# Kernel optimization log

Hardware: AMD Instinct MI355X
Metric: run time of the kernel (lower is better)

## Reference

```python
import jax, jax.numpy as jnp
import numpy as np

B, D, H = 32768, 1024, 8
LN_EPS = 1e-5


def setup_inputs() -> dict:
    key = jax.random.key(0)
    ks = jax.random.split(key, 12)
    w = lambda k, shape: (jax.random.normal(k, shape, dtype=jnp.float32) * 0.02)
    inp = {
        "graph_embedding": jax.random.normal(ks[0], (B, D), dtype=jnp.float32),
        "smiles_embedding": jax.random.normal(ks[1], (B, D), dtype=jnp.float32),
        "num_heads": H,
        # cross_attn_graph_to_smiles params (torch MHA: in_proj [3D,D] split q/k/v, out_proj [D,D])
        "Wq_gs": w(ks[2], (D, D)), "Wk_gs": w(ks[3], (D, D)), "Wv_gs": w(ks[4], (D, D)),
        "bq_gs": jnp.zeros((D,), jnp.float32), "bk_gs": jnp.zeros((D,), jnp.float32), "bv_gs": jnp.zeros((D,), jnp.float32),
        "Wo_gs": w(ks[5], (D, D)), "bo_gs": jnp.zeros((D,), jnp.float32),
        # cross_attn_smiles_to_graph params
        "Wq_sg": w(ks[6], (D, D)), "Wk_sg": w(ks[7], (D, D)), "Wv_sg": w(ks[8], (D, D)),
        "bq_sg": jnp.zeros((D,), jnp.float32), "bk_sg": jnp.zeros((D,), jnp.float32), "bv_sg": jnp.zeros((D,), jnp.float32),
        "Wo_sg": w(ks[9], (D, D)), "bo_sg": jnp.zeros((D,), jnp.float32),
        # LayerNorms
        "ln_g_gamma": jnp.ones((D,), jnp.float32), "ln_g_beta": jnp.zeros((D,), jnp.float32),
        "ln_s_gamma": jnp.ones((D,), jnp.float32), "ln_s_beta": jnp.zeros((D,), jnp.float32),
        # Gate: Linear(2D -> D) then sigmoid
        "Wg": w(ks[10], (D, 2 * D)), "bg": jnp.zeros((D,), jnp.float32),
    }
    return inp


def _layernorm(x, gamma, beta):
    mu = jnp.mean(x, axis=-1, keepdims=True)
    var = jnp.mean(jnp.square(x - mu), axis=-1, keepdims=True)
    return (x - mu) * jax.lax.rsqrt(var + LN_EPS) * gamma + beta


def _mha_len1(kv, Wv, bv, Wo, bo):
    # seq_len=1 cross-attention: softmax over a single key is identically 1,
    # so output == out_proj(v_proj(kv)). q/k projections contribute nothing
    # (and have exactly zero gradient), matching torch's math.
    v = kv @ Wv.T + bv
    return v @ Wo.T + bo


def reference(graph_embedding, smiles_embedding, num_heads,
              Wq_gs, Wk_gs, Wv_gs, bq_gs, bk_gs, bv_gs, Wo_gs, bo_gs,
              Wq_sg, Wk_sg, Wv_sg, bq_sg, bk_sg, bv_sg, Wo_sg, bo_sg,
              ln_g_gamma, ln_g_beta, ln_s_gamma, ln_s_beta, Wg, bg):
    # dropout p=0 / eval mode -> identity
    attn_g2s = _mha_len1(smiles_embedding, Wv_gs, bv_gs, Wo_gs, bo_gs)  # graph queries smiles
    attn_s2g = _mha_len1(graph_embedding, Wv_sg, bv_sg, Wo_sg, bo_sg)   # smiles queries graph
    fused_graph = _layernorm(graph_embedding + attn_g2s, ln_g_gamma, ln_g_beta)
    fused_smiles = _layernorm(smiles_embedding + attn_s2g, ln_s_gamma, ln_s_beta)
    gate_in = jnp.concatenate([fused_graph, fused_smiles], axis=1)  # [B, 2D]
    gate_weight = jax.nn.sigmoid(gate_in @ Wg.T + bg)               # [B, D]
    fused_feature = gate_weight * fused_graph + (1.0 - gate_weight) * fused_smiles
    return fused_feature, gate_weight
```

## Files before the change

kernel.cpp:

```cpp
#include <hip/hip_runtime.h>

#define BROWS 32768
#define DDIM 1024

typedef __bf16 bf16x8v __attribute__((ext_vector_type(8)));
typedef float f32x4v __attribute__((ext_vector_type(4)));

__device__ __forceinline__ float bf2f(unsigned short u) {
  union { unsigned int i; float f; } w; w.i = ((unsigned int)u) << 16; return w.f;
}
__device__ __forceinline__ unsigned short f2bf(float f) {
  union { float f; unsigned int i; } w; w.f = f;
  w.i += 0x7fffu + ((w.i >> 16) & 1u);
  return (unsigned short)(w.i >> 16);
}

__device__ __forceinline__ void gl_lds16(const void* g, void* l) {
  __builtin_amdgcn_global_load_lds((const __attribute__((address_space(1))) void*)g,
                                   (__attribute__((address_space(3))) void*)l, 16, 0, 0);
}

__device__ __forceinline__ int xcd_swz(int bid, int nwg) {
  return (bid & 7) * (nwg >> 3) + (bid >> 3);
}

__device__ __forceinline__ int swzc(int row, int col) {
  return (col & ~63) | ((col & 63) ^ ((row & 7) << 3));
}

__global__ __launch_bounds__(256) void cvt_x(const float* __restrict__ g,
                                             const float* __restrict__ s,
                                             unsigned short* __restrict__ xg,
                                             unsigned short* __restrict__ xs) {
  const size_t N = (size_t)BROWS * DDIM;
  size_t i = ((size_t)blockIdx.x * 256 + threadIdx.x) * 4;
  const float* src = (i < N) ? g : s;
  unsigned short* dst = (i < N) ? xg : xs;
  size_t off = (i < N) ? i : i - N;
  int row = (int)(off >> 10), col = (int)(off & 1023);
  float4 v = *(const float4*)&src[off];
  union { uint2 q; unsigned short h[4]; } u;
  u.h[0] = f2bf(v.x); u.h[1] = f2bf(v.y); u.h[2] = f2bf(v.z); u.h[3] = f2bf(v.w);
  *(uint2*)&dst[(size_t)row * DDIM + swzc(row, col)] = u.q;
}

__global__ __launch_bounds__(256) void cvt_wg(const float* __restrict__ s,
                                              unsigned short* __restrict__ d) {
  int i = (blockIdx.x * 256 + threadIdx.x) * 4;
  int row = i >> 11, col = i & 2047;
  float4 v = *(const float4*)&s[i];
  union { uint2 q; unsigned short h[4]; } u;
  u.h[0] = f2bf(v.x); u.h[1] = f2bf(v.y); u.h[2] = f2bf(v.z); u.h[3] = f2bf(v.w);
  *(uint2*)&d[(size_t)row * 2048 + swzc(row, col)] = u.q;
}

__global__ __launch_bounds__(256) void bias_combine(
    const float* __restrict__ Wo_gs, const float* __restrict__ bv_gs,
    const float* __restrict__ bo_gs,
    const float* __restrict__ Wo_sg, const float* __restrict__ bv_sg,
    const float* __restrict__ bo_sg,
    float* __restrict__ bc_gs, float* __restrict__ bc_sg) {
  int gid = blockIdx.x * 256 + threadIdx.x;
  int pair = gid >> 10, j = gid & 1023;
  const float* Wo = pair ? Wo_sg : Wo_gs;
  const float* bv = pair ? bv_sg : bv_gs;
  const float* bo = pair ? bo_sg : bo_gs;
  float s = 0.f;
  for (int k = 0; k < DDIM; k += 4) {
    float4 w = *(const float4*)&Wo[(size_t)j * DDIM + k];
    float4 b = *(const float4*)&bv[k];
    s += w.x * b.x + w.y * b.y + w.z * b.z + w.w * b.w;
  }
  float* bc = pair ? bc_sg : bc_gs;
  bc[j] = s + bo[j];
}

__device__ __forceinline__ void stage_f32_32(const float* __restrict__ src, int ldk,
                                             int row0, int k0, unsigned short* lds, int tid) {
  const int sr = tid >> 2, sc = (tid & 3) * 8;
#pragma unroll
  for (int h = 0; h < 2; ++h) {
    const float* g = &src[(size_t)(row0 + h * 64 + sr) * ldk + k0 + sc];
    float4 va = ((const float4*)g)[0];
    float4 vb = ((const float4*)g)[1];
    union { uint4 q; unsigned short hh[8]; } u;
    u.hh[0] = f2bf(va.x); u.hh[1] = f2bf(va.y); u.hh[2] = f2bf(va.z); u.hh[3] = f2bf(va.w);
    u.hh[4] = f2bf(vb.x); u.hh[5] = f2bf(vb.y); u.hh[6] = f2bf(vb.z); u.hh[7] = f2bf(vb.w);
    *(uint4*)&lds[(h * 64 + sr) * 32 + sc] = u.q;
  }
}

__device__ __forceinline__ void mfma_tile32(const unsigned short* As, const unsigned short* Bs,
                                            int ab, int bb, f32x4v acc[4][4]) {
  const bf16x8v* Av = reinterpret_cast<const bf16x8v*>(As);
  const bf16x8v* Bv = reinterpret_cast<const bf16x8v*>(Bs);
  bf16x8v af[4], bfr[4];
#pragma unroll
  for (int m = 0; m < 4; ++m) af[m] = Av[ab + m * 64];
#pragma unroll
  for (int n = 0; n < 4; ++n) bfr[n] = Bv[bb + n * 64];
#pragma unroll
  for (int m = 0; m < 4; ++m)
#pragma unroll
    for (int n = 0; n < 4; ++n)
      acc[m][n] = __builtin_amdgcn_mfma_f32_16x16x32_bf16(af[m], bfr[n], acc[m][n], 0, 0, 0);
}

__global__ __launch_bounds__(256) void combine_kernel(
    const float* __restrict__ Wo_gs, const float* __restrict__ Wv_gs,
    const float* __restrict__ Wo_sg, const float* __restrict__ Wv_sg,
    unsigned short* __restrict__ Wc_gs, unsigned short* __restrict__ Wc_sg) {
  const int pair = blockIdx.y;
  const float* Wo = pair ? Wo_sg : Wo_gs;
  const float* Wv = pair ? Wv_sg : Wv_gs;
  unsigned short* Wc = pair ? Wc_sg : Wc_gs;
  const int mt = blockIdx.x >> 3, nt = blockIdx.x & 7;
  const int row0 = mt * 128, col0 = nt * 128;

  __shared__ __align__(16) unsigned short As[128 * 32];
  __shared__ __align__(16) unsigned short Bt[128 * 32];

  const int tid = threadIdx.x;
  const int lane = tid & 63, wave = tid >> 6;
  const int wr = wave >> 1, wc = wave & 1;
  const int lr = lane & 15, lk = lane >> 4;

  f32x4v acc[4][4] = {};
  const int ab = (wr * 64 + lr) * 4 + lk;
  const int bb = (wc * 64 + lr) * 4 + lk;

  for (int tt = 0; tt < 32; ++tt) {
    const int t0 = tt * 32;
    __syncthreads();
    stage_f32_32(Wo, DDIM, row0, t0, As, tid);
#pragma unroll
    for (int h = 0; h < 2; ++h) {
      int chunk = h * 256 + tid;
      int t = chunk >> 4;
      int c8 = (chunk & 15) * 8;
      const float* g = &Wv[(size_t)(t0 + t) * DDIM + col0 + c8];
      float4 va = ((const float4*)g)[0];
      float4 vb = ((const float4*)g)[1];
      float vv[8] = {va.x, va.y, va.z, va.w, vb.x, vb.y, vb.z, vb.w};
#pragma unroll
      for (int e = 0; e < 8; ++e) Bt[(c8 + e) * 32 + t] = f2bf(vv[e]);
    }
    __syncthreads();
    mfma_tile32(As, Bt, ab, bb, acc);
  }

#pragma unroll
  for (int n = 0; n < 4; ++n) {
    int col = col0 + wc * 64 + n * 16 + lr;
#pragma unroll
    for (int m = 0; m < 4; ++m) {
      int rbase = row0 + wr * 64 + m * 16 + lk * 4;
#pragma unroll
      for (int r = 0; r < 4; ++r)
        Wc[(size_t)(rbase + r) * DDIM + swzc(rbase + r, col)] = f2bf(acc[m][n][r]);
    }
  }
}


__global__ __launch_bounds__(512, 2) void gemm_branch8(
    const unsigned short* __restrict__ Xs_b, const unsigned short* __restrict__ Xg_b,
    const unsigned short* __restrict__ Wc_gs, const unsigned short* __restrict__ Wc_sg,
    const float* __restrict__ bc_gs, const float* __restrict__ bc_sg,
    unsigned short* __restrict__ Zg, unsigned short* __restrict__ Zs) {
  const int pair = blockIdx.y;
  const unsigned short* X = pair ? Xg_b : Xs_b;
  const unsigned short* residb = pair ? Xs_b : Xg_b;
  const unsigned short* Wc = pair ? Wc_sg : Wc_gs;
  const float* bc = pair ? bc_sg : bc_gs;
  unsigned short* Z = pair ? Zs : Zg;

  const int bid = xcd_swz(blockIdx.x, 1024);
  const int mt = bid >> 2, nt = bid & 3;
  const int row0 = mt * 128, col0 = nt * 256;
  const int NT = 16;

  __shared__ __align__(16) unsigned short As[4][128 * 64];
  __shared__ __align__(16) unsigned short Bs[2][256 * 64];

  const int tid = threadIdx.x;
  const int lane = tid & 63, wave = tid >> 6;
  const int wm = wave >> 2, wn = wave & 3;
  const int lr = lane & 15, lk = lane >> 4;

  f32x4v acc[4][4] = {};

  auto stageB = [&](int kt, int jj) {
    int idx = jj * 512 + tid, row = idx >> 3, ch = idx & 7;
    gl_lds16(&Wc[(size_t)(col0 + row) * DDIM + kt * 64 + ch * 8], &Bs[kt & 1][idx * 8]);
  };
  auto stageA = [&](int kt, int jj) {
    int idx = jj * 512 + tid, row = idx >> 3, ch = idx & 7;
    gl_lds16(&X[(size_t)(row0 + row) * DDIM + kt * 64 + ch * 8], &As[kt & 3][idx * 8]);
  };

  stageB(0, 0); stageB(0, 1); stageB(0, 2); stageB(0, 3);
  stageA(0, 0); stageA(0, 1);
  stageA(1, 0); stageA(1, 1);
  stageA(2, 0); stageA(2, 1);
  asm volatile("s_waitcnt vmcnt(4)" ::: "memory");
  asm volatile("s_barrier" ::: "memory");

  for (int kt = 0; kt < NT; ++kt) {
    const unsigned short* Ak = As[kt & 3];
    const unsigned short* Bk = Bs[kt & 1];
    bf16x8v bv[4][2];
    {
      bf16x8v av[2][2];
#pragma unroll
      for (int mi = 0; mi < 2; ++mi)
#pragma unroll
        for (int s = 0; s < 2; ++s) {
          int row = wm * 64 + mi * 16 + lr;
          av[mi][s] = *(const bf16x8v*)&Ak[row * 64 + (((s * 4 + lk) ^ (row & 7)) * 8)];
        }
#pragma unroll
      for (int n = 0; n < 4; ++n)
#pragma unroll
        for (int s = 0; s < 2; ++s) {
          int row = wn * 64 + n * 16 + lr;
          bv[n][s] = *(const bf16x8v*)&Bk[row * 64 + (((s * 4 + lk) ^ (row & 7)) * 8)];
        }
      if (kt + 1 < NT) { stageB(kt + 1, 0); stageB(kt + 1, 1); stageB(kt + 1, 2); }
      asm volatile("s_barrier" ::: "memory");
      __builtin_amdgcn_s_setprio(1);
#pragma unroll
      for (int mi = 0; mi < 2; ++mi)
#pragma unroll
        for (int n = 0; n < 4; ++n)
#pragma unroll
          for (int s = 0; s < 2; ++s)
            acc[mi][n] = __builtin_amdgcn_mfma_f32_16x16x32_bf16(av[mi][s], bv[n][s],
                                                                 acc[mi][n], 0, 0, 0);
      __builtin_amdgcn_s_setprio(0);
      asm volatile("s_barrier" ::: "memory");
    }
    {
      bf16x8v av[2][2];
#pragma unroll
      for (int mi = 0; mi < 2; ++mi)
#pragma unroll
        for (int s = 0; s < 2; ++s) {
          int row = wm * 64 + (2 + mi) * 16 + lr;
          av[mi][s] = *(const bf16x8v*)&Ak[row * 64 + (((s * 4 + lk) ^ (row & 7)) * 8)];
        }
      if (kt + 1 < NT) stageB(kt + 1, 3);
      if (kt + 3 < NT) {
        stageA(kt + 3, 0); stageA(kt + 3, 1);
        asm volatile("s_waitcnt vmcnt(2)" ::: "memory");
      } else {
        asm volatile("s_waitcnt vmcnt(0)" ::: "memory");
      }
      asm volatile("s_barrier" ::: "memory");
      __builtin_amdgcn_s_setprio(1);
#pragma unroll
      for (int mi = 0; mi < 2; ++mi)
#pragma unroll
        for (int n = 0; n < 4; ++n)
#pragma unroll
          for (int s = 0; s < 2; ++s)
            acc[2 + mi][n] = __builtin_amdgcn_mfma_f32_16x16x32_bf16(av[mi][s], bv[n][s],
                                                                     acc[2 + mi][n], 0, 0, 0);
      __builtin_amdgcn_s_setprio(0);
      asm volatile("s_barrier" ::: "memory");
    }
  }

#pragma unroll
  for (int n = 0; n < 4; ++n) {
    int col = col0 + wn * 64 + n * 16 + lr;
    float bcv = bc[col];
#pragma unroll
    for (int m = 0; m < 4; ++m) {
      int rb = row0 + wm * 64 + m * 16 + lk * 4;
#pragma unroll
      for (int r = 0; r < 4; ++r) {
        int row = rb + r;
        size_t idx = (size_t)row * DDIM + swzc(row, col);
        Z[idx] = f2bf(acc[m][n][r] + bcv + bf2f(residb[idx]));
      }
    }
  }
}

__global__ __launch_bounds__(512, 2) void gemm_gate8(
    const unsigned short* __restrict__ fg, const unsigned short* __restrict__ fs,
    const unsigned short* __restrict__ WgB, const float* __restrict__ bg,
    float* __restrict__ out0, float* __restrict__ out1) {
  const int bid = xcd_swz(blockIdx.x, 1024);
  const int mt = bid >> 2, nt = bid & 3;
  const int row0 = mt * 128, col0 = nt * 256;
  const int NT = 32;

  __shared__ __align__(16) unsigned short As[4][128 * 64];
  __shared__ __align__(16) unsigned short Bs[2][256 * 64];

  const int tid = threadIdx.x;
  const int lane = tid & 63, wave = tid >> 6;
  const int wm = wave >> 2, wn = wave & 3;
  const int lr = lane & 15, lk = lane >> 4;

  f32x4v acc[4][4] = {};

  auto stageB = [&](int kt, int jj) {
    int idx = jj * 512 + tid, row = idx >> 3, ch = idx & 7;
    gl_lds16(&WgB[(size_t)(col0 + row) * 2048 + kt * 64 + ch * 8], &Bs[kt & 1][idx * 8]);
  };
  auto stageA = [&](int kt, int jj) {
    const unsigned short* asrc = (kt < 16) ? fg : fs;
    int ak0 = (kt & 15) * 64;
    int idx = jj * 512 + tid, row = idx >> 3, ch = idx & 7;
    gl_lds16(&asrc[(size_t)(row0 + row) * DDIM + ak0 + ch * 8], &As[kt & 3][idx * 8]);
  };

  stageB(0, 0); stageB(0, 1); stageB(0, 2); stageB(0, 3);
  stageA(0, 0); stageA(0, 1);
  stageA(1, 0); stageA(1, 1);
  stageA(2, 0); stageA(2, 1);
  asm volatile("s_waitcnt vmcnt(4)" ::: "memory");
  asm volatile("s_barrier" ::: "memory");

  for (int kt = 0; kt < NT; ++kt) {
    const unsigned short* Ak = As[kt & 3];
    const unsigned short* Bk = Bs[kt & 1];
    bf16x8v bv[4][2];
    {
      bf16x8v av[2][2];
#pragma unroll
      for (int mi = 0; mi < 2; ++mi)
#pragma unroll
        for (int s = 0; s < 2; ++s) {
          int row = wm * 64 + mi * 16 + lr;
          av[mi][s] = *(const bf16x8v*)&Ak[row * 64 + (((s * 4 + lk) ^ (row & 7)) * 8)];
        }
#pragma unroll
      for (int n = 0; n < 4; ++n)
#pragma unroll
        for (int s = 0; s < 2; ++s) {
          int row = wn * 64 + n * 16 + lr;
          bv[n][s] = *(const bf16x8v*)&Bk[row * 64 + (((s * 4 + lk) ^ (row & 7)) * 8)];
        }
      if (kt + 1 < NT) { stageB(kt + 1, 0); stageB(kt + 1, 1); stageB(kt + 1, 2); }
      asm volatile("s_barrier" ::: "memory");
      __builtin_amdgcn_s_setprio(1);
#pragma unroll
      for (int mi = 0; mi < 2; ++mi)
#pragma unroll
        for (int n = 0; n < 4; ++n)
#pragma unroll
          for (int s = 0; s < 2; ++s)
            acc[mi][n] = __builtin_amdgcn_mfma_f32_16x16x32_bf16(av[mi][s], bv[n][s],
                                                                 acc[mi][n], 0, 0, 0);
      __builtin_amdgcn_s_setprio(0);
      asm volatile("s_barrier" ::: "memory");
    }
    {
      bf16x8v av[2][2];
#pragma unroll
      for (int mi = 0; mi < 2; ++mi)
#pragma unroll
        for (int s = 0; s < 2; ++s) {
          int row = wm * 64 + (2 + mi) * 16 + lr;
          av[mi][s] = *(const bf16x8v*)&Ak[row * 64 + (((s * 4 + lk) ^ (row & 7)) * 8)];
        }
      if (kt + 1 < NT) stageB(kt + 1, 3);
      if (kt + 3 < NT) {
        stageA(kt + 3, 0); stageA(kt + 3, 1);
        asm volatile("s_waitcnt vmcnt(2)" ::: "memory");
      } else {
        asm volatile("s_waitcnt vmcnt(0)" ::: "memory");
      }
      asm volatile("s_barrier" ::: "memory");
      __builtin_amdgcn_s_setprio(1);
#pragma unroll
      for (int mi = 0; mi < 2; ++mi)
#pragma unroll
        for (int n = 0; n < 4; ++n)
#pragma unroll
          for (int s = 0; s < 2; ++s)
            acc[2 + mi][n] = __builtin_amdgcn_mfma_f32_16x16x32_bf16(av[mi][s], bv[n][s],
                                                                     acc[2 + mi][n], 0, 0, 0);
      __builtin_amdgcn_s_setprio(0);
      asm volatile("s_barrier" ::: "memory");
    }
  }

#pragma unroll
  for (int n = 0; n < 4; ++n) {
    int col = col0 + wn * 64 + n * 16 + lr;
    float bgv = bg[col];
#pragma unroll
    for (int m = 0; m < 4; ++m) {
      int rb = row0 + wm * 64 + m * 16 + lk * 4;
#pragma unroll
      for (int r = 0; r < 4; ++r) {
        int row = rb + r;
        size_t sidx = (size_t)row * DDIM + swzc(row, col);
        size_t tidx = (size_t)row * DDIM + col;
        float g = 1.f / (1.f + __expf(-(acc[m][n][r] + bgv)));
        float a = bf2f(fg[sidx]), b = bf2f(fs[sidx]);
        out0[tidx] = g * a + (1.f - g) * b;
        out1[tidx] = g;
      }
    }
  }
}

__global__ __launch_bounds__(256) void ln_kernel(
    unsigned short* __restrict__ Z,
    const float* __restrict__ gam_g, const float* __restrict__ bet_g,
    const float* __restrict__ gam_s, const float* __restrict__ bet_s) {
  int row = blockIdx.x * 4 + (threadIdx.x >> 6);
  int lane = threadIdx.x & 63;
  const float* gam = (row < BROWS) ? gam_g : gam_s;
  const float* bet = (row < BROWS) ? bet_g : bet_s;
  unsigned short* zr = Z + (size_t)row * DDIM;

  uint4 v0 = *(const uint4*)(zr + lane * 8);
  uint4 v1 = *(const uint4*)(zr + 512 + lane * 8);
  const unsigned short* u0 = (const unsigned short*)&v0;
  const unsigned short* u1 = (const unsigned short*)&v1;
  float x[16];
  float s = 0.f, sq = 0.f;
#pragma unroll
  for (int e = 0; e < 8; ++e) { x[e] = bf2f(u0[e]); x[8 + e] = bf2f(u1[e]); }
#pragma unroll
  for (int i = 0; i < 16; ++i) { s += x[i]; sq += x[i] * x[i]; }
#pragma unroll
  for (int o = 32; o; o >>= 1) { s += __shfl_xor(s, o); sq += __shfl_xor(sq, o); }
  float mu = s * (1.f / 1024.f);
  float var = sq * (1.f / 1024.f) - mu * mu;
  float rstd = rsqrtf(var + 1e-5f);

  int lane2 = (lane & ~7) | ((lane & 7) ^ (row & 7));
  float4 g0 = *(const float4*)(gam + lane2 * 8);
  float4 g1 = *(const float4*)(gam + lane2 * 8 + 4);
  float4 g2 = *(const float4*)(gam + 512 + lane2 * 8);
  float4 g3 = *(const float4*)(gam + 512 + lane2 * 8 + 4);
  float4 b0 = *(const float4*)(bet + lane2 * 8);
  float4 b1 = *(const float4*)(bet + lane2 * 8 + 4);
  float4 b2 = *(const float4*)(bet + 512 + lane2 * 8);
  float4 b3 = *(const float4*)(bet + 512 + lane2 * 8 + 4);
  float gg[16] = {g0.x,g0.y,g0.z,g0.w,g1.x,g1.y,g1.z,g1.w,
                  g2.x,g2.y,g2.z,g2.w,g3.x,g3.y,g3.z,g3.w};
  float bb[16] = {b0.x,b0.y,b0.z,b0.w,b1.x,b1.y,b1.z,b1.w,
                  b2.x,b2.y,b2.z,b2.w,b3.x,b3.y,b3.z,b3.w};

  union { uint4 q; unsigned short h[8]; } o0, o1;
#pragma unroll
  for (int e = 0; e < 8; ++e) {
    o0.h[e] = f2bf((x[e] - mu) * rstd * gg[e] + bb[e]);
    o1.h[e] = f2bf((x[8 + e] - mu) * rstd * gg[8 + e] + bb[8 + e]);
  }
  *(uint4*)(zr + lane * 8) = o0.q;
  *(uint4*)(zr + 512 + lane * 8) = o1.q;
}

__global__ __launch_bounds__(256) void gemm_gate_f32(
    const unsigned short* __restrict__ fg, const unsigned short* __restrict__ fs,
    const float* __restrict__ Wg, const float* __restrict__ bg,
    float* __restrict__ out0, float* __restrict__ out1) {
  const int bid = xcd_swz(blockIdx.x, 2048);
  const int mt = bid >> 3, nt = bid & 7;
  const int row0 = mt * 128, col0 = nt * 128;

  __shared__ __align__(16) unsigned short As[128 * 64];
  __shared__ __align__(16) unsigned short Bsh[128 * 64];

  const int tid = threadIdx.x;
  const int lane = tid & 63, wave = tid >> 6;
  const int wr = wave >> 1, wc = wave & 1;
  const int lr = lane & 15, lk = lane >> 4;

  f32x4v acc[4][4] = {};

  for (int kt = 0; kt < 32; ++kt) {
    const unsigned short* Asrc = (kt < 16) ? fg : fs;
    const int k0 = (kt & 15) * 64;
    const int kw = kt * 64;
    __syncthreads();
#pragma unroll
    for (int h = 0; h < 4; ++h) {
      int row = h * 32 + (tid >> 3);
      gl_lds16(&Asrc[(size_t)(row0 + row) * DDIM + k0 + (tid & 7) * 8], &As[h * 2048 + tid * 8]);
    }
#pragma unroll
    for (int h = 0; h < 4; ++h) {
      int row = h * 32 + (tid >> 3), c16 = tid & 7;
      const float* gsrc = &Wg[(size_t)(col0 + row) * 2048 + kw + c16 * 8];
      float4 va = ((const float4*)gsrc)[0];
      float4 vb = ((const float4*)gsrc)[1];
      union { uint4 q; unsigned short hh[8]; } u;
      u.hh[0] = f2bf(va.x); u.hh[1] = f2bf(va.y); u.hh[2] = f2bf(va.z); u.hh[3] = f2bf(va.w);
      u.hh[4] = f2bf(vb.x); u.hh[5] = f2bf(vb.y); u.hh[6] = f2bf(vb.z); u.hh[7] = f2bf(vb.w);
      *(uint4*)&Bsh[(row * 8 + (c16 ^ (row & 7))) * 8] = u.q;
    }
    __syncthreads();
    const bf16x8v* Av = reinterpret_cast<const bf16x8v*>(As);
    const bf16x8v* Bv = reinterpret_cast<const bf16x8v*>(Bsh);
    const int xr = lr & 7;
#pragma unroll
    for (int s = 0; s < 2; ++s) {
      const int u = (s * 4 + lk) ^ xr;
      bf16x8v af[4], bfr[4];
#pragma unroll
      for (int m = 0; m < 4; ++m) af[m] = Av[(wr * 64 + m * 16 + lr) * 8 + u];
#pragma unroll
      for (int n = 0; n < 4; ++n) bfr[n] = Bv[(wc * 64 + n * 16 + lr) * 8 + u];
#pragma unroll
      for (int m = 0; m < 4; ++m)
#pragma unroll
        for (int n = 0; n < 4; ++n)
          acc[m][n] = __builtin_amdgcn_mfma_f32_16x16x32_bf16(af[m], bfr[n], acc[m][n], 0, 0, 0);
    }
  }

#pragma unroll
  for (int n = 0; n < 4; ++n) {
    int col = col0 + wc * 64 + n * 16 + lr;
    float bgv = bg[col];
#pragma unroll
    for (int m = 0; m < 4; ++m) {
      int rbase = row0 + wr * 64 + m * 16 + lk * 4;
#pragma unroll
      for (int r = 0; r < 4; ++r) {
        int row = rbase + r;
        size_t sidx = (size_t)row * DDIM + swzc(row, col);
        size_t tidx = (size_t)row * DDIM + col;
        float g = 1.f / (1.f + __expf(-(acc[m][n][r] + bgv)));
        float a = bf2f(fg[sidx]), b = bf2f(fs[sidx]);
        out0[tidx] = g * a + (1.f - g) * b;
        out1[tidx] = g;
      }
    }
  }
}

extern "C" void kernel_launch(void* const* d_in, const int* in_sizes, int n_in,
                              void* d_out, int out_size, void* d_ws, size_t ws_size,
                              hipStream_t stream) {
  const float* graph  = (const float*)d_in[0];
  const float* smiles = (const float*)d_in[1];
  const float* Wv_gs  = (const float*)d_in[5];
  const float* bv_gs  = (const float*)d_in[8];
  const float* Wo_gs  = (const float*)d_in[9];
  const float* bo_gs  = (const float*)d_in[10];
  const float* Wv_sg  = (const float*)d_in[13];
  const float* bv_sg  = (const float*)d_in[16];
  const float* Wo_sg  = (const float*)d_in[17];
  const float* bo_sg  = (const float*)d_in[18];
  const float* ln_gg  = (const float*)d_in[19];
  const float* ln_gb  = (const float*)d_in[20];
  const float* ln_sg  = (const float*)d_in[21];
  const float* ln_sb  = (const float*)d_in[22];
  const float* Wg     = (const float*)d_in[23];
  const float* bg     = (const float*)d_in[24];

  char* ob = (char*)d_out;
  unsigned short* Xg_b  = (unsigned short*)ob;
  unsigned short* Xs_b  = (unsigned short*)(ob + (64u << 20));
  unsigned short* Wc_gs = (unsigned short*)(ob + (128u << 20));
  unsigned short* Wc_sg = (unsigned short*)(ob + (130u << 20));
  float* bc_gs = (float*)(ob + (132u << 20));
  float* bc_sg = (float*)(ob + (132u << 20) + 4096);

  unsigned short* Zg = (unsigned short*)d_ws;
  unsigned short* Zs = Zg + (size_t)BROWS * DDIM;
  const bool fast = ws_size >= ((size_t)132 << 20);
  unsigned short* WgB = (unsigned short*)((char*)d_ws + ((size_t)128 << 20));

  float* out0 = (float*)d_out;
  float* out1 = out0 + (size_t)BROWS * DDIM;

  cvt_x<<<dim3(65536), dim3(256), 0, stream>>>(graph, smiles, Xg_b, Xs_b);
  bias_combine<<<dim3(8), dim3(256), 0, stream>>>(Wo_gs, bv_gs, bo_gs, Wo_sg, bv_sg, bo_sg,
                                                  bc_gs, bc_sg);
  combine_kernel<<<dim3(64, 2), dim3(256), 0, stream>>>(Wo_gs, Wv_gs, Wo_sg, Wv_sg,
                                                        Wc_gs, Wc_sg);
  if (fast) cvt_wg<<<dim3(2048), dim3(256), 0, stream>>>(Wg, WgB);
  gemm_branch8<<<dim3(1024, 2), dim3(512), 0, stream>>>(Xs_b, Xg_b, Wc_gs, Wc_sg,
                                                        bc_gs, bc_sg, Zg, Zs);
  ln_kernel<<<dim3(16384), dim3(256), 0, stream>>>(Zg, ln_gg, ln_gb, ln_sg, ln_sb);
  if (fast)
    gemm_gate8<<<dim3(1024), dim3(512), 0, stream>>>(Zg, Zs, WgB, bg, out0, out1);
  else
    gemm_gate_f32<<<dim3(2048), dim3(256), 0, stream>>>(Zg, Zs, Wg, bg, out0, out1);
}
```

Baseline: 756.1 us.

## Enlarge GEMM tiles to 256x256 with double-buffered A and four-phase pipeline

Both bf16 GEMM kernels (branch and gate) move from 128x256 to 256x256 output tiles per block, halving the grid and doubling the accumulators per wave. The A buffer changes from a 4-deep 128-row ring to a 2-deep 256-row ring. B fragments are now loaded once per k-step, and the loop is split into four phases that interleave next-step B and A loads with MFMA work. The aim is more reuse per global byte and fewer redundant B loads. In exchange, register pressure rises (32 accumulators per lane) under launch_bounds(512,2), which may cause spills or lower occupancy, and prefetch depth is shallower.

```diff
diff --git a/kernel.cpp b/kernel.cpp
--- a/kernel.cpp
+++ b/kernel.cpp
@@ -163,6 +163,7 @@
 }
 
 
+
 __global__ __launch_bounds__(512, 2) void gemm_branch8(
     const unsigned short* __restrict__ Xs_b, const unsigned short* __restrict__ Xg_b,
     const unsigned short* __restrict__ Wc_gs, const unsigned short* __restrict__ Wc_sg,
@@ -175,12 +176,12 @@
   const float* bc = pair ? bc_sg : bc_gs;
   unsigned short* Z = pair ? Zs : Zg;
 
-  const int bid = xcd_swz(blockIdx.x, 1024);
+  const int bid = xcd_swz(blockIdx.x, 512);
   const int mt = bid >> 2, nt = bid & 3;
-  const int row0 = mt * 128, col0 = nt * 256;
+  const int row0 = mt * 256, col0 = nt * 256;
   const int NT = 16;
 
-  __shared__ __align__(16) unsigned short As[4][128 * 64];
+  __shared__ __align__(16) unsigned short As[2][256 * 64];
   __shared__ __align__(16) unsigned short Bs[2][256 * 64];
 
   const int tid = threadIdx.x;
@@ -188,45 +189,54 @@
   const int wm = wave >> 2, wn = wave & 3;
   const int lr = lane & 15, lk = lane >> 4;
 
-  f32x4v acc[4][4] = {};
-
+  f32x4v acc[8][4] = {};
+
+  auto stageA = [&](int kt, int jj) {
+    int idx = jj * 512 + tid, row = idx >> 3, ch = idx & 7;
+    gl_lds16(&X[(size_t)(row0 + row) * DDIM + kt * 64 + ch * 8], &As[kt & 1][idx * 8]);
+  };
   auto stageB = [&](int kt, int jj) {
     int idx = jj * 512 + tid, row = idx >> 3, ch = idx & 7;
     gl_lds16(&Wc[(size_t)(col0 + row) * DDIM + kt * 64 + ch * 8], &Bs[kt & 1][idx * 8]);
   };
-  auto stageA = [&](int kt, int jj) {
-    int idx = jj * 512 + tid, row = idx >> 3, ch = idx & 7;
-    gl_lds16(&X[(size_t)(row0 + row) * DDIM + kt * 64 + ch * 8], &As[kt & 3][idx * 8]);
-  };
 
   stageB(0, 0); stageB(0, 1); stageB(0, 2); stageB(0, 3);
-  stageA(0, 0); stageA(0, 1);
-  stageA(1, 0); stageA(1, 1);
-  stageA(2, 0); stageA(2, 1);
-  asm volatile("s_waitcnt vmcnt(4)" ::: "memory");
+  stageA(0, 0); stageA(0, 2);
+  stageA(0, 1); stageA(0, 3);
+  asm volatile("s_waitcnt vmcnt(2)" ::: "memory");
   asm volatile("s_barrier" ::: "memory");
 
   for (int kt = 0; kt < NT; ++kt) {
-    const unsigned short* Ak = As[kt & 3];
+    const unsigned short* Ak = As[kt & 1];
     const unsigned short* Bk = Bs[kt & 1];
     bf16x8v bv[4][2];
-    {
+#pragma unroll
+    for (int n = 0; n < 4; ++n)
+#pragma unroll
+      for (int s = 0; s < 2; ++s) {
+        int row = wn * 64 + n * 16 + lr;
+        bv[n][s] = *(const bf16x8v*)&Bk[row * 64 + (((s * 4 + lk) ^ (row & 7)) * 8)];
+      }
+#pragma unroll
+    for (int ph = 0; ph < 4; ++ph) {
       bf16x8v av[2][2];
 #pragma unroll
       for (int mi = 0; mi < 2; ++mi)
 #pragma unroll
         for (int s = 0; s < 2; ++s) {
-          int row = wm * 64 + mi * 16 + lr;
+          int row = wm * 128 + (ph * 2 + mi) * 16 + lr;
           av[mi][s] = *(const bf16x8v*)&Ak[row * 64 + (((s * 4 + lk) ^ (row & 7)) * 8)];
         }
-#pragma unroll
-      for (int n = 0; n < 4; ++n)
-#pragma unroll
-        for (int s = 0; s < 2; ++s) {
-          int row = wn * 64 + n * 16 + lr;
-          bv[n][s] = *(const bf16x8v*)&Bk[row * 64 + (((s * 4 + lk) ^ (row & 7)) * 8)];
-        }
-      if (kt + 1 < NT) { stageB(kt + 1, 0); stageB(kt + 1, 1); stageB(kt + 1, 2); }
+      if (kt + 1 < NT) {
+        if (ph == 0) { stageB(kt + 1, 0); stageB(kt + 1, 1); }
+        else if (ph == 1) { stageB(kt + 1, 2); stageB(kt + 1, 3);
+                            asm volatile("s_waitcnt vmcnt(4)" ::: "memory"); }
+        else if (ph == 2) { stageA(kt + 1, 0); stageA(kt + 1, 2); }
+        else { stageA(kt + 1, 1); stageA(kt + 1, 3);
+               asm volatile("s_waitcnt vmcnt(2)" ::: "memory"); }
+      } else {
+        if (ph == 1) asm volatile("s_waitcnt vmcnt(0)" ::: "memory");
+      }
       asm volatile("s_barrier" ::: "memory");
       __builtin_amdgcn_s_setprio(1);
 #pragma unroll
@@ -235,37 +245,8 @@
         for (int n = 0; n < 4; ++n)
 #pragma unroll
           for (int s = 0; s < 2; ++s)
-            acc[mi][n] = __builtin_amdgcn_mfma_f32_16x16x32_bf16(av[mi][s], bv[n][s],
-                                                                 acc[mi][n], 0, 0, 0);
-      __builtin_amdgcn_s_setprio(0);
-      asm volatile("s_barrier" ::: "memory");
-    }
-    {
-      bf16x8v av[2][2];
-#pragma unroll
-      for (int mi = 0; mi < 2; ++mi)
-#pragma unroll
-        for (int s = 0; s < 2; ++s) {
-          int row = wm * 64 + (2 + mi) * 16 + lr;
-          av[mi][s] = *(const bf16x8v*)&Ak[row * 64 + (((s * 4 + lk) ^ (row & 7)) * 8)];
-        }
-      if (kt + 1 < NT) stageB(kt + 1, 3);
-      if (kt + 3 < NT) {
-        stageA(kt + 3, 0); stageA(kt + 3, 1);
-        asm volatile("s_waitcnt vmcnt(2)" ::: "memory");
-      } else {
-        asm volatile("s_waitcnt vmcnt(0)" ::: "memory");
-      }
-      asm volatile("s_barrier" ::: "memory");
-      __builtin_amdgcn_s_setprio(1);
-#pragma unroll
-      for (int mi = 0; mi < 2; ++mi)
-#pragma unroll
-        for (int n = 0; n < 4; ++n)
-#pragma unroll
-          for (int s = 0; s < 2; ++s)
-            acc[2 + mi][n] = __builtin_amdgcn_mfma_f32_16x16x32_bf16(av[mi][s], bv[n][s],
-                                                                     acc[2 + mi][n], 0, 0, 0);
+            acc[ph * 2 + mi][n] = __builtin_amdgcn_mfma_f32_16x16x32_bf16(
+                av[mi][s], bv[n][s], acc[ph * 2 + mi][n], 0, 0, 0);
       __builtin_amdgcn_s_setprio(0);
       asm volatile("s_barrier" ::: "memory");
     }
@@ -276,8 +257,8 @@
     int col = col0 + wn * 64 + n * 16 + lr;
     float bcv = bc[col];
 #pragma unroll
-    for (int m = 0; m < 4; ++m) {
-      int rb = row0 + wm * 64 + m * 16 + lk * 4;
+    for (int m = 0; m < 8; ++m) {
+      int rb = row0 + wm * 128 + m * 16 + lk * 4;
 #pragma unroll
       for (int r = 0; r < 4; ++r) {
         int row = rb + r;
@@ -292,12 +273,12 @@
     const unsigned short* __restrict__ fg, const unsigned short* __restrict__ fs,
     const unsigned short* __restrict__ WgB, const float* __restrict__ bg,
     float* __restrict__ out0, float* __restrict__ out1) {
-  const int bid = xcd_swz(blockIdx.x, 1024);
+  const int bid = xcd_swz(blockIdx.x, 512);
   const int mt = bid >> 2, nt = bid & 3;
-  const int row0 = mt * 128, col0 = nt * 256;
+  const int row0 = mt * 256, col0 = nt * 256;
   const int NT = 32;
 
-  __shared__ __align__(16) unsigned short As[4][128 * 64];
+  __shared__ __align__(16) unsigned short As[2][256 * 64];
   __shared__ __align__(16) unsigned short Bs[2][256 * 64];
 
   const int tid = threadIdx.x;
@@ -305,47 +286,56 @@
   const int wm = wave >> 2, wn = wave & 3;
   const int lr = lane & 15, lk = lane >> 4;
 
-  f32x4v acc[4][4] = {};
-
+  f32x4v acc[8][4] = {};
+
+  auto stageA = [&](int kt, int jj) {
+    const unsigned short* asrc = (kt < 16) ? fg : fs;
+    int ak0 = (kt & 15) * 64;
+    int idx = jj * 512 + tid, row = idx >> 3, ch = idx & 7;
+    gl_lds16(&asrc[(size_t)(row0 + row) * DDIM + ak0 + ch * 8], &As[kt & 1][idx * 8]);
+  };
   auto stageB = [&](int kt, int jj) {
     int idx = jj * 512 + tid, row = idx >> 3, ch = idx & 7;
     gl_lds16(&WgB[(size_t)(col0 + row) * 2048 + kt * 64 + ch * 8], &Bs[kt & 1][idx * 8]);
   };
-  auto stageA = [&](int kt, int jj) {
-    const unsigned short* asrc = (kt < 16) ? fg : fs;
-    int ak0 = (kt & 15) * 64;
-    int idx = jj * 512 + tid, row = idx >> 3, ch = idx & 7;
-    gl_lds16(&asrc[(size_t)(row0 + row) * DDIM + ak0 + ch * 8], &As[kt & 3][idx * 8]);
-  };
 
   stageB(0, 0); stageB(0, 1); stageB(0, 2); stageB(0, 3);
-  stageA(0, 0); stageA(0, 1);
-  stageA(1, 0); stageA(1, 1);
-  stageA(2, 0); stageA(2, 1);
-  asm volatile("s_waitcnt vmcnt(4)" ::: "memory");
+  stageA(0, 0); stageA(0, 2);
+  stageA(0, 1); stageA(0, 3);
+  asm volatile("s_waitcnt vmcnt(2)" ::: "memory");
   asm volatile("s_barrier" ::: "memory");
 
   for (int kt = 0; kt < NT; ++kt) {
-    const unsigned short* Ak = As[kt & 3];
+    const unsigned short* Ak = As[kt & 1];
     const unsigned short* Bk = Bs[kt & 1];
     bf16x8v bv[4][2];
-    {
+#pragma unroll
+    for (int n = 0; n < 4; ++n)
+#pragma unroll
+      for (int s = 0; s < 2; ++s) {
+        int row = wn * 64 + n * 16 + lr;
+        bv[n][s] = *(const bf16x8v*)&Bk[row * 64 + (((s * 4 + lk) ^ (row & 7)) * 8)];
+      }
+#pragma unroll
+    for (int ph = 0; ph < 4; ++ph) {
       bf16x8v av[2][2];
 #pragma unroll
       for (int mi = 0; mi < 2; ++mi)
 #pragma unroll
         for (int s = 0; s < 2; ++s) {
-          int row = wm * 64 + mi * 16 + lr;
+          int row = wm * 128 + (ph * 2 + mi) * 16 + lr;
           av[mi][s] = *(const bf16x8v*)&Ak[row * 64 + (((s * 4 + lk) ^ (row & 7)) * 8)];
         }
-#pragma unroll
-      for (int n = 0; n < 4; ++n)
-#pragma unroll
-        for (int s = 0; s < 2; ++s) {
-          int row = wn * 64 + n * 16 + lr;
-          bv[n][s] = *(const bf16x8v*)&Bk[row * 64 + (((s * 4 + lk) ^ (row & 7)) * 8)];
-        }
-      if (kt + 1 < NT) { stageB(kt + 1, 0); stageB(kt + 1, 1); stageB(kt + 1, 2); }
+      if (kt + 1 < NT) {
+        if (ph == 0) { stageB(kt + 1, 0); stageB(kt + 1, 1); }
+        else if (ph == 1) { stageB(kt + 1, 2); stageB(kt + 1, 3);
+                            asm volatile("s_waitcnt vmcnt(4)" ::: "memory"); }
+        else if (ph == 2) { stageA(kt + 1, 0); stageA(kt + 1, 2); }
+        else { stageA(kt + 1, 1); stageA(kt + 1, 3);
+               asm volatile("s_waitcnt vmcnt(2)" ::: "memory"); }
+      } else {
+        if (ph == 1) asm volatile("s_waitcnt vmcnt(0)" ::: "memory");
+      }
       asm volatile("s_barrier" ::: "memory");
       __builtin_amdgcn_s_setprio(1);
 #pragma unroll
@@ -354,37 +344,8 @@
         for (int n = 0; n < 4; ++n)
 #pragma unroll
           for (int s = 0; s < 2; ++s)
-            acc[mi][n] = __builtin_amdgcn_mfma_f32_16x16x32_bf16(av[mi][s], bv[n][s],
-                                                                 acc[mi][n], 0, 0, 0);
-      __builtin_amdgcn_s_setprio(0);
-      asm volatile("s_barrier" ::: "memory");
-    }
-    {
-      bf16x8v av[2][2];
-#pragma unroll
-      for (int mi = 0; mi < 2; ++mi)
-#pragma unroll
-        for (int s = 0; s < 2; ++s) {
-          int row = wm * 64 + (2 + mi) * 16 + lr;
-          av[mi][s] = *(const bf16x8v*)&Ak[row * 64 + (((s * 4 + lk) ^ (row & 7)) * 8)];
-        }
-      if (kt + 1 < NT) stageB(kt + 1, 3);
-      if (kt + 3 < NT) {
-        stageA(kt + 3, 0); stageA(kt + 3, 1);
-        asm volatile("s_waitcnt vmcnt(2)" ::: "memory");
-      } else {
-        asm volatile("s_waitcnt vmcnt(0)" ::: "memory");
-      }
-      asm volatile("s_barrier" ::: "memory");
-      __builtin_amdgcn_s_setprio(1);
-#pragma unroll
-      for (int mi = 0; mi < 2; ++mi)
-#pragma unroll
-        for (int n = 0; n < 4; ++n)
-#pragma unroll
-          for (int s = 0; s < 2; ++s)
-            acc[2 + mi][n] = __builtin_amdgcn_mfma_f32_16x16x32_bf16(av[mi][s], bv[n][s],
-                                                                     acc[2 + mi][n], 0, 0, 0);
+            acc[ph * 2 + mi][n] = __builtin_amdgcn_mfma_f32_16x16x32_bf16(
+                av[mi][s], bv[n][s], acc[ph * 2 + mi][n], 0, 0, 0);
       __builtin_amdgcn_s_setprio(0);
       asm volatile("s_barrier" ::: "memory");
     }
@@ -395,8 +356,8 @@
     int col = col0 + wn * 64 + n * 16 + lr;
     float bgv = bg[col];
 #pragma unroll
-    for (int m = 0; m < 4; ++m) {
-      int rb = row0 + wm * 64 + m * 16 + lk * 4;
+    for (int m = 0; m < 8; ++m) {
+      int rb = row0 + wm * 128 + m * 16 + lk * 4;
 #pragma unroll
       for (int r = 0; r < 4; ++r) {
         int row = rb + r;
@@ -583,11 +544,11 @@
   combine_kernel<<<dim3(64, 2), dim3(256), 0, stream>>>(Wo_gs, Wv_gs, Wo_sg, Wv_sg,
                                                         Wc_gs, Wc_sg);
   if (fast) cvt_wg<<<dim3(2048), dim3(256), 0, stream>>>(Wg, WgB);
-  gemm_branch8<<<dim3(1024, 2), dim3(512), 0, stream>>>(Xs_b, Xg_b, Wc_gs, Wc_sg,
-                                                        bc_gs, bc_sg, Zg, Zs);
+  gemm_branch8<<<dim3(512, 2), dim3(512), 0, stream>>>(Xs_b, Xg_b, Wc_gs, Wc_sg,
+                                                       bc_gs, bc_sg, Zg, Zs);
   ln_kernel<<<dim3(16384), dim3(256), 0, stream>>>(Zg, ln_gg, ln_gb, ln_sg, ln_sb);
   if (fast)
-    gemm_gate8<<<dim3(1024), dim3(512), 0, stream>>>(Zg, Zs, WgB, bg, out0, out1);
+    gemm_gate8<<<dim3(512), dim3(512), 0, stream>>>(Zg, Zs, WgB, bg, out0, out1);
   else
     gemm_gate_f32<<<dim3(2048), dim3(256), 0, stream>>>(Zg, Zs, Wg, bg, out0, out1);
 }
```

New measurement: 817.1 us. 8.1% more time.

## Collapse two-phase GEMM k-loop into one barrier per k-step

Applied to the files above, without the earlier changes.

Both bf16 MFMA GEMM kernels previously split each 64-wide k-step into two half-phases with four s_barriers and interleaved global-to-LDS staging. The loop now waits once on vmcnt, hits a single barrier, issues all prefetches for B(kt+1) and A(kt+3), then loads all A/B fragments and runs the full 4x4x2 MFMA block. This cuts barrier stalls and simplifies the schedule. In exchange it holds more fragment registers at once and loses the finer interleaving of LDS reads with MFMA work.

```diff
diff --git a/kernel.cpp b/kernel.cpp
--- a/kernel.cpp
+++ b/kernel.cpp
@@ -203,72 +203,43 @@
   stageA(0, 0); stageA(0, 1);
   stageA(1, 0); stageA(1, 1);
   stageA(2, 0); stageA(2, 1);
-  asm volatile("s_waitcnt vmcnt(4)" ::: "memory");
-  asm volatile("s_barrier" ::: "memory");
 
   for (int kt = 0; kt < NT; ++kt) {
+    if (kt == 0)          asm volatile("s_waitcnt vmcnt(4)" ::: "memory");
+    else if (kt < NT - 3) asm volatile("s_waitcnt vmcnt(2)" ::: "memory");
+    else                  asm volatile("s_waitcnt vmcnt(0)" ::: "memory");
+    asm volatile("s_barrier" ::: "memory");
+    if (kt + 1 < NT) { stageB(kt + 1, 0); stageB(kt + 1, 1);
+                       stageB(kt + 1, 2); stageB(kt + 1, 3); }
+    if (kt + 3 < NT) { stageA(kt + 3, 0); stageA(kt + 3, 1); }
+
     const unsigned short* Ak = As[kt & 3];
     const unsigned short* Bk = Bs[kt & 1];
-    bf16x8v bv[4][2];
-    {
-      bf16x8v av[2][2];
-#pragma unroll
-      for (int mi = 0; mi < 2; ++mi)
-#pragma unroll
-        for (int s = 0; s < 2; ++s) {
-          int row = wm * 64 + mi * 16 + lr;
-          av[mi][s] = *(const bf16x8v*)&Ak[row * 64 + (((s * 4 + lk) ^ (row & 7)) * 8)];
-        }
-#pragma unroll
-      for (int n = 0; n < 4; ++n)
-#pragma unroll
-        for (int s = 0; s < 2; ++s) {
-          int row = wn * 64 + n * 16 + lr;
-          bv[n][s] = *(const bf16x8v*)&Bk[row * 64 + (((s * 4 + lk) ^ (row & 7)) * 8)];
-        }
-      if (kt + 1 < NT) { stageB(kt + 1, 0); stageB(kt + 1, 1); stageB(kt + 1, 2); }
-      asm volatile("s_barrier" ::: "memory");
-      __builtin_amdgcn_s_setprio(1);
-#pragma unroll
-      for (int mi = 0; mi < 2; ++mi)
+    bf16x8v bv[4][2], av[4][2];
+#pragma unroll
+    for (int n = 0; n < 4; ++n)
+#pragma unroll
+      for (int s = 0; s < 2; ++s) {
+        int row = wn * 64 + n * 16 + lr;
+        bv[n][s] = *(const bf16x8v*)&Bk[row * 64 + (((s * 4 + lk) ^ (row & 7)) * 8)];
+      }
+#pragma unroll
+    for (int m = 0; m < 4; ++m)
+#pragma unroll
+      for (int s = 0; s < 2; ++s) {
+        int row = wm * 64 + m * 16 + lr;
+        av[m][s] = *(const bf16x8v*)&Ak[row * 64 + (((s * 4 + lk) ^ (row & 7)) * 8)];
+      }
+    __builtin_amdgcn_s_setprio(1);
+#pragma unroll
+    for (int s = 0; s < 2; ++s)
+#pragma unroll
+      for (int m = 0; m < 4; ++m)
 #pragma unroll
         for (int n = 0; n < 4; ++n)
-#pragma unroll
-          for (int s = 0; s < 2; ++s)
-            acc[mi][n] = __builtin_amdgcn_mfma_f32_16x16x32_bf16(av[mi][s], bv[n][s],
-                                                                 acc[mi][n], 0, 0, 0);
-      __builtin_amdgcn_s_setprio(0);
-      asm volatile("s_barrier" ::: "memory");
-    }
-    {
-      bf16x8v av[2][2];
-#pragma unroll
-      for (int mi = 0; mi < 2; ++mi)
-#pragma unroll
-        for (int s = 0; s < 2; ++s) {
-          int row = wm * 64 + (2 + mi) * 16 + lr;
-          av[mi][s] = *(const bf16x8v*)&Ak[row * 64 + (((s * 4 + lk) ^ (row & 7)) * 8)];
-        }
-      if (kt + 1 < NT) stageB(kt + 1, 3);
-      if (kt + 3 < NT) {
-        stageA(kt + 3, 0); stageA(kt + 3, 1);
-        asm volatile("s_waitcnt vmcnt(2)" ::: "memory");
-      } else {
-        asm volatile("s_waitcnt vmcnt(0)" ::: "memory");
-      }
-      asm volatile("s_barrier" ::: "memory");
-      __builtin_amdgcn_s_setprio(1);
-#pragma unroll
-      for (int mi = 0; mi < 2; ++mi)
-#pragma unroll
-        for (int n = 0; n < 4; ++n)
-#pragma unroll
-          for (int s = 0; s < 2; ++s)
-            acc[2 + mi][n] = __builtin_amdgcn_mfma_f32_16x16x32_bf16(av[mi][s], bv[n][s],
-                                                                     acc[2 + mi][n], 0, 0, 0);
-      __builtin_amdgcn_s_setprio(0);
-      asm volatile("s_barrier" ::: "memory");
-    }
+          acc[m][n] = __builtin_amdgcn_mfma_f32_16x16x32_bf16(av[m][s], bv[n][s],
+                                                              acc[m][n], 0, 0, 0);
+    __builtin_amdgcn_s_setprio(0);
   }
 
 #pragma unroll
@@ -322,72 +293,43 @@
   stageA(0, 0); stageA(0, 1);
   stageA(1, 0); stageA(1, 1);
   stageA(2, 0); stageA(2, 1);
-  asm volatile("s_waitcnt vmcnt(4)" ::: "memory");
-  asm volatile("s_barrier" ::: "memory");
 
   for (int kt = 0; kt < NT; ++kt) {
+    if (kt == 0)          asm volatile("s_waitcnt vmcnt(4)" ::: "memory");
+    else if (kt < NT - 3) asm volatile("s_waitcnt vmcnt(2)" ::: "memory");
+    else                  asm volatile("s_waitcnt vmcnt(0)" ::: "memory");
+    asm volatile("s_barrier" ::: "memory");
+    if (kt + 1 < NT) { stageB(kt + 1, 0); stageB(kt + 1, 1);
+                       stageB(kt + 1, 2); stageB(kt + 1, 3); }
+    if (kt + 3 < NT) { stageA(kt + 3, 0); stageA(kt + 3, 1); }
+
     const unsigned short* Ak = As[kt & 3];
     const unsigned short* Bk = Bs[kt & 1];
-    bf16x8v bv[4][2];
-    {
-      bf16x8v av[2][2];
-#pragma unroll
-      for (int mi = 0; mi < 2; ++mi)
-#pragma unroll
-        for (int s = 0; s < 2; ++s) {
-          int row = wm * 64 + mi * 16 + lr;
-          av[mi][s] = *(const bf16x8v*)&Ak[row * 64 + (((s * 4 + lk) ^ (row & 7)) * 8)];
-        }
-#pragma unroll
-      for (int n = 0; n < 4; ++n)
-#pragma unroll
-        for (int s = 0; s < 2; ++s) {
-          int row = wn * 64 + n * 16 + lr;
-          bv[n][s] = *(const bf16x8v*)&Bk[row * 64 + (((s * 4 + lk) ^ (row & 7)) * 8)];
-        }
-      if (kt + 1 < NT) { stageB(kt + 1, 0); stageB(kt + 1, 1); stageB(kt + 1, 2); }
-      asm volatile("s_barrier" ::: "memory");
-      __builtin_amdgcn_s_setprio(1);
-#pragma unroll
-      for (int mi = 0; mi < 2; ++mi)
+    bf16x8v bv[4][2], av[4][2];
+#pragma unroll
+    for (int n = 0; n < 4; ++n)
+#pragma unroll
+      for (int s = 0; s < 2; ++s) {
+        int row = wn * 64 + n * 16 + lr;
+        bv[n][s] = *(const bf16x8v*)&Bk[row * 64 + (((s * 4 + lk) ^ (row & 7)) * 8)];
+      }
+#pragma unroll
+    for (int m = 0; m < 4; ++m)
+#pragma unroll
+      for (int s = 0; s < 2; ++s) {
+        int row = wm * 64 + m * 16 + lr;
+        av[m][s] = *(const bf16x8v*)&Ak[row * 64 + (((s * 4 + lk) ^ (row & 7)) * 8)];
+      }
+    __builtin_amdgcn_s_setprio(1);
+#pragma unroll
+    for (int s = 0; s < 2; ++s)
+#pragma unroll
+      for (int m = 0; m < 4; ++m)
 #pragma unroll
         for (int n = 0; n < 4; ++n)
-#pragma unroll
-          for (int s = 0; s < 2; ++s)
-            acc[mi][n] = __builtin_amdgcn_mfma_f32_16x16x32_bf16(av[mi][s], bv[n][s],
-                                                                 acc[mi][n], 0, 0, 0);
-      __builtin_amdgcn_s_setprio(0);
-      asm volatile("s_barrier" ::: "memory");
-    }
-    {
-      bf16x8v av[2][2];
-#pragma unroll
-      for (int mi = 0; mi < 2; ++mi)
-#pragma unroll
-        for (int s = 0; s < 2; ++s) {
-          int row = wm * 64 + (2 + mi) * 16 + lr;
-          av[mi][s] = *(const bf16x8v*)&Ak[row * 64 + (((s * 4 + lk) ^ (row & 7)) * 8)];
-        }
-      if (kt + 1 < NT) stageB(kt + 1, 3);
-      if (kt + 3 < NT) {
-        stageA(kt + 3, 0); stageA(kt + 3, 1);
-        asm volatile("s_waitcnt vmcnt(2)" ::: "memory");
-      } else {
-        asm volatile("s_waitcnt vmcnt(0)" ::: "memory");
-      }
-      asm volatile("s_barrier" ::: "memory");
-      __builtin_amdgcn_s_setprio(1);
-#pragma unroll
-      for (int mi = 0; mi < 2; ++mi)
-#pragma unroll
-        for (int n = 0; n < 4; ++n)
-#pragma unroll
-          for (int s = 0; s < 2; ++s)
-            acc[2 + mi][n] = __builtin_amdgcn_mfma_f32_16x16x32_bf16(av[mi][s], bv[n][s],
-                                                                     acc[2 + mi][n], 0, 0, 0);
-      __builtin_amdgcn_s_setprio(0);
-      asm volatile("s_barrier" ::: "memory");
-    }
+          acc[m][n] = __builtin_amdgcn_mfma_f32_16x16x32_bf16(av[m][s], bv[n][s],
+                                                              acc[m][n], 0, 0, 0);
+    __builtin_amdgcn_s_setprio(0);
   }
 
 #pragma unroll
```

New measurement: 765.5 us. Within noise of the previous version (+1.2%).
